# Kernel optimization log

Measured on AMD Instinct MI355X. Metric: run time of the kernel, lower is better.

## Reference

```python
import jax, jax.numpy as jnp
import numpy as np

B, T, C = 2, 2048, 1024
H = 16
D = C // H  # head_dim = 64
SCALE = D ** -0.5


def setup_inputs() -> dict:
    key = jax.random.key(0)
    ks = jax.random.split(key, 5)
    x = jax.random.normal(ks[0], (B, T, C), dtype=jnp.float32)
    # causal mask: -inf above diagonal, 0 elsewhere (module checks mask == -inf)
    neg_inf = jnp.float32(-jnp.inf)
    causal = jnp.where(jnp.tril(jnp.ones((T, T), dtype=bool)), 0.0, neg_inf)
    mask = causal[None, None, :, :].astype(jnp.float32)  # [1,1,T,T]
    # xavier_normal for [C, C] linear weights: std = sqrt(2/(C+C))
    std = float(np.sqrt(2.0 / (C + C)))
    wq = jax.random.normal(ks[1], (C, C), dtype=jnp.float32) * std
    wk = jax.random.normal(ks[2], (C, C), dtype=jnp.float32) * std
    wv = jax.random.normal(ks[3], (C, C), dtype=jnp.float32) * std
    wo = jax.random.normal(ks[4], (C, C), dtype=jnp.float32) * std
    return {"x": x, "mask": mask, "wq": wq, "wk": wk, "wv": wv, "wo": wo}


def reference(x, mask, wq, wk, wv, wo):
    # torch nn.Linear: y = x @ W.T
    q = jnp.einsum('btc,oc->bto', x, wq).reshape(B, T, H, D).transpose(0, 2, 1, 3)
    k = jnp.einsum('btc,oc->bto', x, wk).reshape(B, T, H, D).transpose(0, 2, 1, 3)
    v = jnp.einsum('btc,oc->bto', x, wv).reshape(B, T, H, D).transpose(0, 2, 1, 3)
    scores = jnp.einsum('bhqd,bhkd->bhqk', q, k) * SCALE  # [B,H,T,T]
    scores = jnp.where(mask == -jnp.inf, -jnp.inf, scores)
    attn = jax.nn.softmax(scores, axis=-1)
    out = jnp.einsum('bhqk,bhkd->bhqd', attn, v)  # [B,H,T,D]
    out = out.transpose(0, 2, 1, 3).reshape(B, T, C)
    return jnp.einsum('btc,oc->bto', out, wo)
```

## Files before the change

### kernel.cpp

```cpp
#include <hip/hip_runtime.h>
#include <hip/hip_bf16.h>


typedef __bf16 bf16_t;
typedef __bf16 bf16x8 __attribute__((ext_vector_type(8)));
typedef __bf16 bf16x4 __attribute__((ext_vector_type(4)));
typedef __bf16 bf16x2 __attribute__((ext_vector_type(2)));
typedef float  f32x4  __attribute__((ext_vector_type(4)));
typedef unsigned u32x4 __attribute__((ext_vector_type(4)));

__device__ __forceinline__ void gload_lds16(const bf16_t* g, bf16_t* l) {
  __builtin_amdgcn_global_load_lds((__attribute__((address_space(1))) void*)g,
                                   (__attribute__((address_space(3))) void*)l, 16, 0, 0);
}

__device__ __forceinline__ unsigned pack_bf16(float a, float b) {
  bf16x2 v; v[0] = (bf16_t)a; v[1] = (bf16_t)b;
  return __builtin_bit_cast(unsigned, v);
}

__global__ __launch_bounds__(256) void cvt_all(
    const float* __restrict__ x,  const float* __restrict__ i0, const float* __restrict__ i1,
    const float* __restrict__ i2, const float* __restrict__ i3,
    bf16_t* __restrict__ ox, bf16_t* __restrict__ o0, bf16_t* __restrict__ o1,
    bf16_t* __restrict__ o2, bf16_t* __restrict__ o3) {
  int blk = blockIdx.x;
  const float* in; bf16_t* out; int i;
  if (blk < 4096) { in = x; out = ox; i = blk * 256 + threadIdx.x; }
  else {
    int wb = blk - 4096;
    int which = wb >> 10;
    in  = (which == 0) ? i0 : (which == 1) ? i1 : (which == 2) ? i2 : i3;
    out = (which == 0) ? o0 : (which == 1) ? o1 : (which == 2) ? o2 : o3;
    i = (wb & 1023) * 256 + threadIdx.x;
  }
  float4 v = reinterpret_cast<const float4*>(in)[i];
  bf16x4 o;
  o[0] = (bf16_t)v.x; o[1] = (bf16_t)v.y; o[2] = (bf16_t)v.z; o[3] = (bf16_t)v.w;
  reinterpret_cast<bf16x4*>(out)[i] = o;
}

#define TM 128
#define TN 128
#define TK 64

__global__ __launch_bounds__(256) void gemm_bt(
    const bf16_t* __restrict__ A,
    const bf16_t* __restrict__ W0, const bf16_t* __restrict__ W1, const bf16_t* __restrict__ W2,
    bf16_t* __restrict__ O0, bf16_t* __restrict__ O1, bf16_t* __restrict__ O2,
    float* __restrict__ OF, int kind)
{
  __shared__ alignas(16) bf16_t As[TM * TK];
  __shared__ alignas(16) bf16_t Bs[TN * TK];
  const int K = 1024;
  const int t = threadIdx.x;
  const int lane = t & 63;
  const int w = t >> 6;
  const int wr = w >> 1, wc = w & 1;
  const int lo = lane & 15, hi = lane >> 4;
  const int m0 = blockIdx.x * TM, n0 = blockIdx.y * TN;

  int mode;
  const bf16_t* Bw;
  bf16_t* outb = nullptr;
  if (kind == 1) { mode = 3; Bw = W0; }
  else {
    mode = blockIdx.z;
    Bw   = (mode == 0) ? W0 : (mode == 1) ? W1 : W2;
    outb = (mode == 0) ? O0 : (mode == 1) ? O1 : O2;
  }

  f32x4 acc[4][4] = {};
  const int srow = t >> 3;
  const int sch  = t & 7;

  for (int k0 = 0; k0 < K; k0 += TK) {
#pragma unroll
    for (int r = 0; r < 4; ++r) {
      int row = r * 32 + srow;
      gload_lds16(A  + (size_t)(m0 + row) * K + k0 + sch * 8, &As[row * TK + sch * 8]);
      gload_lds16(Bw + (size_t)(n0 + row) * K + k0 + sch * 8, &Bs[row * TK + sch * 8]);
    }
    __syncthreads();
#pragma unroll
    for (int ks = 0; ks < 2; ++ks) {
      bf16x8 af[4], bfr[4];
#pragma unroll
      for (int i = 0; i < 4; ++i) {
        af[i]  = *reinterpret_cast<const bf16x8*>(&As[(wr * 64 + i * 16 + lo) * TK + ks * 32 + hi * 8]);
        bfr[i] = *reinterpret_cast<const bf16x8*>(&Bs[(wc * 64 + i * 16 + lo) * TK + ks * 32 + hi * 8]);
      }
#pragma unroll
      for (int i = 0; i < 4; ++i)
#pragma unroll
        for (int j = 0; j < 4; ++j)
          acc[i][j] = __builtin_amdgcn_mfma_f32_16x16x32_bf16(af[i], bfr[j], acc[i][j], 0, 0, 0);
    }
    __syncthreads();
  }

  if (mode == 2) {
#pragma unroll
    for (int i = 0; i < 4; ++i)
#pragma unroll
      for (int j = 0; j < 4; ++j) {
        int m = m0 + wr * 64 + i * 16 + hi * 4;
        int n = n0 + wc * 64 + j * 16 + lo;
        int b = m >> 11, tq = m & 2047;
        int h = (n >> 6) & 15, d = n & 63;
        bf16x4 pk;
#pragma unroll
        for (int r = 0; r < 4; ++r) pk[r] = (bf16_t)acc[i][j][r];
        *reinterpret_cast<bf16x4*>(
            &outb[((size_t)(b * 16 + h) * 64 + d) * 2048 + tq]) = pk;
      }
  } else {
#pragma unroll
    for (int i = 0; i < 4; ++i)
#pragma unroll
      for (int j = 0; j < 4; ++j)
#pragma unroll
        for (int r = 0; r < 4; ++r) {
          int m = m0 + wr * 64 + i * 16 + hi * 4 + r;
          int n = n0 + wc * 64 + j * 16 + lo;
          float v = acc[i][j][r];
          if (mode == 3) {
            OF[(size_t)m * 1024 + n] = v;
          } else {
            int b = m >> 11, tq = m & 2047;
            int h = n >> 6,  d  = n & 63;
            if (mode == 0) v *= 0.18033688011f;
            outb[((size_t)(b * 16 + h) * 2048 + tq) * 64 + d] = (bf16_t)v;
          }
        }
  }
}

#define SLAB 8832

__global__ __launch_bounds__(256) void attn_fwd(
    const bf16_t* __restrict__ Q,
    const bf16_t* __restrict__ Km,
    const bf16_t* __restrict__ Vt,
    bf16_t* __restrict__ att)
{
  __shared__ alignas(16) char smem[4 * SLAB];
  const int t = threadIdx.x, lane = t & 63, w = t >> 6;
  const int lo = lane & 15, h = lane >> 4;
  const int blk = blockIdx.x;
  const int item = (blk & 7) * 128 + (blk >> 3);
  const int bh = item >> 5;
  const int pr = item & 31;
  const bf16_t* Qb = Q  + (size_t)bh * 2048 * 64;
  const bf16_t* Kb = Km + (size_t)bh * 2048 * 64;
  const bf16_t* Vb = Vt + (size_t)bh * 64 * 2048;
  float* accW = (float*)(smem + w * SLAB);
  float* lW   = (float*)(smem + w * SLAB + 8704);
  const int b = bh >> 4, hd = bh & 15;
  const int src1 = lo + 32 * (h & 1);
  const int src2 = src1 + 16;
  const bool hsel = (h >> 1) != 0;

  auto run_tile = [&](int q0) {
    bf16x8 qf[2][2];
#pragma unroll
    for (int qt = 0; qt < 2; ++qt)
#pragma unroll
      for (int ks = 0; ks < 2; ++ks)
        qf[qt][ks] = *reinterpret_cast<const bf16x8*>(
            &Qb[(size_t)(q0 + qt * 16 + lo) * 64 + ks * 32 + h * 8]);

    f32x4 acc[2][4] = {};
    float lp[2] = {};
    const int kend = q0 + 32;
    for (int kb = w * 64; kb < kend; kb += 256) {
      f32x4 s_t[4][2] = {};
#pragma unroll
      for (int ks = 0; ks < 2; ++ks) {
        bf16x8 kf[4];
#pragma unroll
        for (int kt = 0; kt < 4; ++kt)
          kf[kt] = *reinterpret_cast<const bf16x8*>(
              &Kb[(size_t)(kb + kt * 16 + lo) * 64 + ks * 32 + h * 8]);
        __builtin_amdgcn_s_setprio(1);
#pragma unroll
        for (int kt = 0; kt < 4; ++kt)
#pragma unroll
          for (int qt = 0; qt < 2; ++qt)
            s_t[kt][qt] = __builtin_amdgcn_mfma_f32_16x16x32_bf16(kf[kt], qf[qt][ks], s_t[kt][qt], 0, 0, 0);
        __builtin_amdgcn_s_setprio(0);
      }
      bf16x8 vf[2][4];
#pragma unroll
      for (int kh = 0; kh < 2; ++kh)
#pragma unroll
        for (int dt = 0; dt < 4; ++dt)
          vf[kh][dt] = *reinterpret_cast<const bf16x8*>(
              &Vb[(size_t)(dt * 16 + lo) * 2048 + kb + kh * 32 + h * 8]);
      if (kb + 63 >= q0) {
#pragma unroll
        for (int kt = 0; kt < 4; ++kt)
#pragma unroll
          for (int qt = 0; qt < 2; ++qt)
#pragma unroll
            for (int r = 0; r < 4; ++r) {
              int kg = kb + kt * 16 + h * 4 + r;
              int qg = q0 + qt * 16 + lo;
              if (kg > qg) s_t[kt][qt][r] = -__builtin_inff();
            }
      }
      unsigned uP[2][4][2];
#pragma unroll
      for (int qt = 0; qt < 2; ++qt)
#pragma unroll
        for (int kt = 0; kt < 4; ++kt) {
          float p0 = exp2f(s_t[kt][qt][0]);
          float p1 = exp2f(s_t[kt][qt][1]);
          float p2 = exp2f(s_t[kt][qt][2]);
          float p3 = exp2f(s_t[kt][qt][3]);
          lp[qt] += (p0 + p1) + (p2 + p3);
          uP[qt][kt][0] = pack_bf16(p0, p1);
          uP[qt][kt][1] = pack_bf16(p2, p3);
        }
#pragma unroll
      for (int kh = 0; kh < 2; ++kh)
#pragma unroll
        for (int qt = 0; qt < 2; ++qt) {
          unsigned a0x = __shfl((int)uP[qt][2 * kh][0], src1);
          unsigned a0y = __shfl((int)uP[qt][2 * kh + 1][0], src1);
          unsigned a1x = __shfl((int)uP[qt][2 * kh][1], src1);
          unsigned a1y = __shfl((int)uP[qt][2 * kh + 1][1], src1);
          unsigned a2x = __shfl((int)uP[qt][2 * kh][0], src2);
          unsigned a2y = __shfl((int)uP[qt][2 * kh + 1][0], src2);
          unsigned a3x = __shfl((int)uP[qt][2 * kh][1], src2);
          unsigned a3y = __shfl((int)uP[qt][2 * kh + 1][1], src2);
          u32x4 au;
          au[0] = hsel ? a0y : a0x;
          au[1] = hsel ? a1y : a1x;
          au[2] = hsel ? a2y : a2x;
          au[3] = hsel ? a3y : a3x;
          bf16x8 pa = __builtin_bit_cast(bf16x8, au);
          __builtin_amdgcn_s_setprio(1);
#pragma unroll
          for (int dt = 0; dt < 4; ++dt)
            acc[qt][dt] = __builtin_amdgcn_mfma_f32_16x16x32_bf16(pa, vf[kh][dt], acc[qt][dt], 0, 0, 0);
          __builtin_amdgcn_s_setprio(0);
        }
    }

    float lrow[2];
#pragma unroll
    for (int qt = 0; qt < 2; ++qt) {
      float v = lp[qt];
      v += __shfl_xor(v, 16);
      v += __shfl_xor(v, 32);
      lrow[qt] = v;
    }

#pragma unroll
    for (int qt = 0; qt < 2; ++qt) {
#pragma unroll
      for (int r = 0; r < 4; ++r) {
        int row = qt * 16 + h * 4 + r;
#pragma unroll
        for (int dt = 0; dt < 4; ++dt)
          accW[row * 68 + dt * 16 + lo] = acc[qt][dt][r];
      }
      if (h == 0) lW[qt * 16 + lo] = lrow[qt];
    }
    __syncthreads();

    {
      const int row = t >> 3, c0 = (t & 7) * 8;
      float lsum = 0.f, o[8] = {};
#pragma unroll
      for (int w2 = 0; w2 < 4; ++w2) {
        lsum += ((const float*)(smem + w2 * SLAB + 8704))[row];
        const float* a2 = (const float*)(smem + w2 * SLAB) + row * 68 + c0;
#pragma unroll
        for (int j = 0; j < 8; ++j) o[j] += a2[j];
      }
      float inv = 1.f / lsum;
      bf16x8 ov;
#pragma unroll
      for (int j = 0; j < 8; ++j) ov[j] = (bf16_t)(o[j] * inv);
      *reinterpret_cast<bf16x8*>(&att[((size_t)(b * 2048 + q0 + row)) * 1024 + hd * 64 + c0]) = ov;
    }
    __syncthreads();
  };

  run_tile((63 - pr) * 32);
  run_tile(pr * 32);
}

extern "C" void kernel_launch(void* const* d_in, const int* in_sizes, int n_in,
                              void* d_out, int out_size, void* d_ws, size_t ws_size,
                              hipStream_t stream) {
  (void)in_sizes; (void)n_in; (void)out_size; (void)ws_size;
  const float* x  = (const float*)d_in[0];
  const float* wq = (const float*)d_in[2];
  const float* wk = (const float*)d_in[3];
  const float* wv = (const float*)d_in[4];
  const float* wo = (const float*)d_in[5];
  float* out = (float*)d_out;

  char* ws = (char*)d_ws;
  const size_t SZ_X = (size_t)4096 * 1024 * 2;
  const size_t SZ_W = (size_t)1024 * 1024 * 2;
  bf16_t* xb  = (bf16_t*)(ws);
  bf16_t* wqb = (bf16_t*)(ws + SZ_X);
  bf16_t* wkb = (bf16_t*)(ws + SZ_X + 1 * SZ_W);
  bf16_t* wvb = (bf16_t*)(ws + SZ_X + 2 * SZ_W);
  bf16_t* wob = (bf16_t*)(ws + SZ_X + 3 * SZ_W);
  bf16_t* qw  = (bf16_t*)(ws + 1 * SZ_X + 4 * SZ_W);
  bf16_t* kw  = (bf16_t*)(ws + 2 * SZ_X + 4 * SZ_W);
  bf16_t* vtw = (bf16_t*)(ws + 3 * SZ_X + 4 * SZ_W);
  bf16_t* att = xb;

  cvt_all<<<8192, 256, 0, stream>>>(x, wq, wk, wv, wo, xb, wqb, wkb, wvb, wob);

  gemm_bt<<<dim3(32, 8, 3), 256, 0, stream>>>(xb, wqb, wkb, wvb, qw, kw, vtw, nullptr, 0);
  attn_fwd<<<1024, 256, 0, stream>>>(qw, kw, vtw, att);
  gemm_bt<<<dim3(32, 8, 1), 256, 0, stream>>>(att, wob, nullptr, nullptr,
                                              nullptr, nullptr, nullptr, out, 1);
}
```

Baseline: 155.6 us.

## Double-buffer GEMM LDS tiles, hoist attention K/V loads, use native exp2

The projection GEMM now uses two LDS buffers, issuing async global-to-LDS loads for the next K tile before computing the current one, with explicit vmcnt waits and raw barriers. This is meant to hide global load latency behind MFMA work. In attention, all K and V fragment loads are issued before the QK MFMAs so memory latency overlaps compute. exp2f is replaced by the hardware exp2 builtin to drop range handling. The changes double LDS use in the GEMM and add register pressure in attention.

```diff
diff --git a/kernel.cpp b/kernel.cpp
--- a/kernel.cpp
+++ b/kernel.cpp
@@ -18,6 +18,8 @@
   bf16x2 v; v[0] = (bf16_t)a; v[1] = (bf16_t)b;
   return __builtin_bit_cast(unsigned, v);
 }
+
+__device__ __forceinline__ float fexp2(float x) { return __builtin_amdgcn_exp2f(x); }
 
 __global__ __launch_bounds__(256) void cvt_all(
     const float* __restrict__ x,  const float* __restrict__ i0, const float* __restrict__ i1,
@@ -50,9 +52,9 @@
     bf16_t* __restrict__ O0, bf16_t* __restrict__ O1, bf16_t* __restrict__ O2,
     float* __restrict__ OF, int kind)
 {
-  __shared__ alignas(16) bf16_t As[TM * TK];
-  __shared__ alignas(16) bf16_t Bs[TN * TK];
-  const int K = 1024;
+  __shared__ alignas(16) bf16_t As[2][TM * TK];
+  __shared__ alignas(16) bf16_t Bs[2][TN * TK];
+  const int K = 1024, NT = K / TK;
   const int t = threadIdx.x;
   const int lane = t & 63;
   const int w = t >> 6;
@@ -74,21 +76,32 @@
   const int srow = t >> 3;
   const int sch  = t & 7;
 
-  for (int k0 = 0; k0 < K; k0 += TK) {
+  auto stage = [&](int buf, int k0) {
 #pragma unroll
     for (int r = 0; r < 4; ++r) {
       int row = r * 32 + srow;
-      gload_lds16(A  + (size_t)(m0 + row) * K + k0 + sch * 8, &As[row * TK + sch * 8]);
-      gload_lds16(Bw + (size_t)(n0 + row) * K + k0 + sch * 8, &Bs[row * TK + sch * 8]);
-    }
-    __syncthreads();
+      gload_lds16(A  + (size_t)(m0 + row) * K + k0 + sch * 8, &As[buf][row * TK + sch * 8]);
+      gload_lds16(Bw + (size_t)(n0 + row) * K + k0 + sch * 8, &Bs[buf][row * TK + sch * 8]);
+    }
+  };
+
+  stage(0, 0);
+  for (int ti = 0; ti < NT; ++ti) {
+    const int cur = ti & 1;
+    if (ti + 1 < NT) {
+      stage(cur ^ 1, (ti + 1) * TK);
+      asm volatile("s_waitcnt vmcnt(8)" ::: "memory");
+    } else {
+      asm volatile("s_waitcnt vmcnt(0)" ::: "memory");
+    }
+    __builtin_amdgcn_s_barrier();
 #pragma unroll
     for (int ks = 0; ks < 2; ++ks) {
       bf16x8 af[4], bfr[4];
 #pragma unroll
       for (int i = 0; i < 4; ++i) {
-        af[i]  = *reinterpret_cast<const bf16x8*>(&As[(wr * 64 + i * 16 + lo) * TK + ks * 32 + hi * 8]);
-        bfr[i] = *reinterpret_cast<const bf16x8*>(&Bs[(wc * 64 + i * 16 + lo) * TK + ks * 32 + hi * 8]);
+        af[i]  = *reinterpret_cast<const bf16x8*>(&As[cur][(wr * 64 + i * 16 + lo) * TK + ks * 32 + hi * 8]);
+        bfr[i] = *reinterpret_cast<const bf16x8*>(&Bs[cur][(wc * 64 + i * 16 + lo) * TK + ks * 32 + hi * 8]);
       }
 #pragma unroll
       for (int i = 0; i < 4; ++i)
@@ -96,7 +109,7 @@
         for (int j = 0; j < 4; ++j)
           acc[i][j] = __builtin_amdgcn_mfma_f32_16x16x32_bf16(af[i], bfr[j], acc[i][j], 0, 0, 0);
     }
-    __syncthreads();
+    __builtin_amdgcn_s_barrier();
   }
 
   if (mode == 2) {
@@ -174,22 +187,13 @@
     float lp[2] = {};
     const int kend = q0 + 32;
     for (int kb = w * 64; kb < kend; kb += 256) {
-      f32x4 s_t[4][2] = {};
-#pragma unroll
-      for (int ks = 0; ks < 2; ++ks) {
-        bf16x8 kf[4];
+      bf16x8 kf[2][4];
+#pragma unroll
+      for (int ks = 0; ks < 2; ++ks)
 #pragma unroll
         for (int kt = 0; kt < 4; ++kt)
-          kf[kt] = *reinterpret_cast<const bf16x8*>(
+          kf[ks][kt] = *reinterpret_cast<const bf16x8*>(
               &Kb[(size_t)(kb + kt * 16 + lo) * 64 + ks * 32 + h * 8]);
-        __builtin_amdgcn_s_setprio(1);
-#pragma unroll
-        for (int kt = 0; kt < 4; ++kt)
-#pragma unroll
-          for (int qt = 0; qt < 2; ++qt)
-            s_t[kt][qt] = __builtin_amdgcn_mfma_f32_16x16x32_bf16(kf[kt], qf[qt][ks], s_t[kt][qt], 0, 0, 0);
-        __builtin_amdgcn_s_setprio(0);
-      }
       bf16x8 vf[2][4];
 #pragma unroll
       for (int kh = 0; kh < 2; ++kh)
@@ -197,6 +201,17 @@
         for (int dt = 0; dt < 4; ++dt)
           vf[kh][dt] = *reinterpret_cast<const bf16x8*>(
               &Vb[(size_t)(dt * 16 + lo) * 2048 + kb + kh * 32 + h * 8]);
+      f32x4 s_t[4][2] = {};
+#pragma unroll
+      for (int ks = 0; ks < 2; ++ks) {
+        __builtin_amdgcn_s_setprio(1);
+#pragma unroll
+        for (int kt = 0; kt < 4; ++kt)
+#pragma unroll
+          for (int qt = 0; qt < 2; ++qt)
+            s_t[kt][qt] = __builtin_amdgcn_mfma_f32_16x16x32_bf16(kf[ks][kt], qf[qt][ks], s_t[kt][qt], 0, 0, 0);
+        __builtin_amdgcn_s_setprio(0);
+      }
       if (kb + 63 >= q0) {
 #pragma unroll
         for (int kt = 0; kt < 4; ++kt)
@@ -214,10 +229,10 @@
       for (int qt = 0; qt < 2; ++qt)
 #pragma unroll
         for (int kt = 0; kt < 4; ++kt) {
-          float p0 = exp2f(s_t[kt][qt][0]);
-          float p1 = exp2f(s_t[kt][qt][1]);
-          float p2 = exp2f(s_t[kt][qt][2]);
-          float p3 = exp2f(s_t[kt][qt][3]);
+          float p0 = fexp2(s_t[kt][qt][0]);
+          float p1 = fexp2(s_t[kt][qt][1]);
+          float p2 = fexp2(s_t[kt][qt][2]);
+          float p3 = fexp2(s_t[kt][qt][3]);
           lp[qt] += (p0 + p1) + (p2 + p3);
           uP[qt][kt][0] = pack_bf16(p0, p1);
           uP[qt][kt][1] = pack_bf16(p2, p3);
```

Result: slower. 160.7 us (+3.3%).

## Permute K row order so softmax probabilities feed PV MFMA without shuffles

Applied to the files above, without the earlier changes.

Loads K rows in a permuted order so each lane's QK^T MFMA output lands directly in the A-operand layout the PV MFMA expects. This removes the eight cross-lane shuffles and selects per P fragment. It also switches to the raw hardware exp2 builtin, hoists the V loads ahead of the score MFMAs, and drops the s_setprio hints. The causal-mask index math is updated to match the new row order, which correctness now depends on.

```diff
diff --git a/kernel.cpp b/kernel.cpp
--- a/kernel.cpp
+++ b/kernel.cpp
@@ -18,6 +18,8 @@
   bf16x2 v; v[0] = (bf16_t)a; v[1] = (bf16_t)b;
   return __builtin_bit_cast(unsigned, v);
 }
+
+__device__ __forceinline__ float fexp2(float x) { return __builtin_amdgcn_exp2f(x); }
 
 __global__ __launch_bounds__(256) void cvt_all(
     const float* __restrict__ x,  const float* __restrict__ i0, const float* __restrict__ i1,
@@ -157,9 +159,7 @@
   float* accW = (float*)(smem + w * SLAB);
   float* lW   = (float*)(smem + w * SLAB + 8704);
   const int b = bh >> 4, hd = bh & 15;
-  const int src1 = lo + 32 * (h & 1);
-  const int src2 = src1 + 16;
-  const bool hsel = (h >> 1) != 0;
+  const int prow = 8 * (lo >> 2) + (lo & 3);
 
   auto run_tile = [&](int q0) {
     bf16x8 qf[2][2];
@@ -174,22 +174,15 @@
     float lp[2] = {};
     const int kend = q0 + 32;
     for (int kb = w * 64; kb < kend; kb += 256) {
-      f32x4 s_t[4][2] = {};
-#pragma unroll
-      for (int ks = 0; ks < 2; ++ks) {
-        bf16x8 kf[4];
-#pragma unroll
-        for (int kt = 0; kt < 4; ++kt)
-          kf[kt] = *reinterpret_cast<const bf16x8*>(
-              &Kb[(size_t)(kb + kt * 16 + lo) * 64 + ks * 32 + h * 8]);
-        __builtin_amdgcn_s_setprio(1);
-#pragma unroll
-        for (int kt = 0; kt < 4; ++kt)
-#pragma unroll
-          for (int qt = 0; qt < 2; ++qt)
-            s_t[kt][qt] = __builtin_amdgcn_mfma_f32_16x16x32_bf16(kf[kt], qf[qt][ks], s_t[kt][qt], 0, 0, 0);
-        __builtin_amdgcn_s_setprio(0);
-      }
+      bf16x8 kf[2][4];
+#pragma unroll
+      for (int ks = 0; ks < 2; ++ks)
+#pragma unroll
+        for (int kt = 0; kt < 4; ++kt) {
+          int krow = kb + 32 * (kt & 1) + 4 * (kt >> 1) + prow;
+          kf[ks][kt] = *reinterpret_cast<const bf16x8*>(
+              &Kb[(size_t)krow * 64 + ks * 32 + h * 8]);
+        }
       bf16x8 vf[2][4];
 #pragma unroll
       for (int kh = 0; kh < 2; ++kh)
@@ -197,6 +190,14 @@
         for (int dt = 0; dt < 4; ++dt)
           vf[kh][dt] = *reinterpret_cast<const bf16x8*>(
               &Vb[(size_t)(dt * 16 + lo) * 2048 + kb + kh * 32 + h * 8]);
+      f32x4 s_t[4][2] = {};
+#pragma unroll
+      for (int ks = 0; ks < 2; ++ks)
+#pragma unroll
+        for (int kt = 0; kt < 4; ++kt)
+#pragma unroll
+          for (int qt = 0; qt < 2; ++qt)
+            s_t[kt][qt] = __builtin_amdgcn_mfma_f32_16x16x32_bf16(kf[ks][kt], qf[qt][ks], s_t[kt][qt], 0, 0, 0);
       if (kb + 63 >= q0) {
 #pragma unroll
         for (int kt = 0; kt < 4; ++kt)
@@ -204,47 +205,34 @@
           for (int qt = 0; qt < 2; ++qt)
 #pragma unroll
             for (int r = 0; r < 4; ++r) {
-              int kg = kb + kt * 16 + h * 4 + r;
+              int kg = kb + 32 * (kt & 1) + 8 * h + 4 * (kt >> 1) + r;
               int qg = q0 + qt * 16 + lo;
               if (kg > qg) s_t[kt][qt][r] = -__builtin_inff();
             }
       }
-      unsigned uP[2][4][2];
-#pragma unroll
-      for (int qt = 0; qt < 2; ++qt)
-#pragma unroll
-        for (int kt = 0; kt < 4; ++kt) {
-          float p0 = exp2f(s_t[kt][qt][0]);
-          float p1 = exp2f(s_t[kt][qt][1]);
-          float p2 = exp2f(s_t[kt][qt][2]);
-          float p3 = exp2f(s_t[kt][qt][3]);
-          lp[qt] += (p0 + p1) + (p2 + p3);
-          uP[qt][kt][0] = pack_bf16(p0, p1);
-          uP[qt][kt][1] = pack_bf16(p2, p3);
-        }
-#pragma unroll
-      for (int kh = 0; kh < 2; ++kh)
+#pragma unroll
+      for (int kt = 0; kt < 4; ++kt)
+#pragma unroll
+        for (int qt = 0; qt < 2; ++qt)
+#pragma unroll
+          for (int r = 0; r < 4; ++r) {
+            float p = fexp2(s_t[kt][qt][r]);
+            s_t[kt][qt][r] = p;
+            lp[qt] += p;
+          }
+#pragma unroll
+      for (int ks2 = 0; ks2 < 2; ++ks2)
 #pragma unroll
         for (int qt = 0; qt < 2; ++qt) {
-          unsigned a0x = __shfl((int)uP[qt][2 * kh][0], src1);
-          unsigned a0y = __shfl((int)uP[qt][2 * kh + 1][0], src1);
-          unsigned a1x = __shfl((int)uP[qt][2 * kh][1], src1);
-          unsigned a1y = __shfl((int)uP[qt][2 * kh + 1][1], src1);
-          unsigned a2x = __shfl((int)uP[qt][2 * kh][0], src2);
-          unsigned a2y = __shfl((int)uP[qt][2 * kh + 1][0], src2);
-          unsigned a3x = __shfl((int)uP[qt][2 * kh][1], src2);
-          unsigned a3y = __shfl((int)uP[qt][2 * kh + 1][1], src2);
           u32x4 au;
-          au[0] = hsel ? a0y : a0x;
-          au[1] = hsel ? a1y : a1x;
-          au[2] = hsel ? a2y : a2x;
-          au[3] = hsel ? a3y : a3x;
+          au[0] = pack_bf16(s_t[ks2][qt][0], s_t[ks2][qt][1]);
+          au[1] = pack_bf16(s_t[ks2][qt][2], s_t[ks2][qt][3]);
+          au[2] = pack_bf16(s_t[ks2 + 2][qt][0], s_t[ks2 + 2][qt][1]);
+          au[3] = pack_bf16(s_t[ks2 + 2][qt][2], s_t[ks2 + 2][qt][3]);
           bf16x8 pa = __builtin_bit_cast(bf16x8, au);
-          __builtin_amdgcn_s_setprio(1);
 #pragma unroll
           for (int dt = 0; dt < 4; ++dt)
-            acc[qt][dt] = __builtin_amdgcn_mfma_f32_16x16x32_bf16(pa, vf[kh][dt], acc[qt][dt], 0, 0, 0);
-          __builtin_amdgcn_s_setprio(0);
+            acc[qt][dt] = __builtin_amdgcn_mfma_f32_16x16x32_bf16(pa, vf[ks2][dt], acc[qt][dt], 0, 0, 0);
         }
     }
 
```

Measured after the change: 154.6 us. Within noise of the previous version (-0.7%).
